# Kernel optimization log

Hardware: AMD Instinct MI355X
Metric: run time of the kernel (lower is better)

## Reference

```python
import jax, jax.numpy as jnp
import numpy as np

K = 16
EPS = 1e-5
NEG_SLOPE = 0.2


def leaky(x):
    return jnp.where(x > 0, x, NEG_SLOPE * x)


def batchnorm_train(x, gamma, beta):
    # x: [B, D]; training-mode BN with biased variance (torch semantics)
    mean = jnp.mean(x, axis=0)
    var = jnp.mean((x - mean) ** 2, axis=0)
    return (x - mean) * jax.lax.rsqrt(var + EPS) * gamma + beta


def setup_inputs() -> dict:
    key = jax.random.key(0)
    ks = jax.random.split(key, 20)
    N, M, D = 30000, 8000, 16
    s = lambda fan_in: 1.0 / np.sqrt(fan_in)
    inp = {
        "xyz": jax.random.normal(ks[0], (N, 3), jnp.float32),
        "atom_xyz": jax.random.normal(ks[1], (M, 3), jnp.float32),
        "atom_types": jax.random.normal(ks[2], (M, D), jnp.float32),
        "Wt1": jax.random.uniform(ks[3], (D, D), jnp.float32, -s(D), s(D)),
        "bt1": jax.random.uniform(ks[4], (D,), jnp.float32, -s(D), s(D)),
        "Wt2": jax.random.uniform(ks[5], (D, D), jnp.float32, -s(D), s(D)),
        "bt2": jax.random.uniform(ks[6], (D,), jnp.float32, -s(D), s(D)),
        "Wt3": jax.random.uniform(ks[7], (D, D), jnp.float32, -s(D), s(D)),
        "bt3": jax.random.uniform(ks[8], (D,), jnp.float32, -s(D), s(D)),
        # embed: conv1 Linear(D+1, D), conv2 Linear(D, D), conv3 Linear(2D, D)
        "W1": jax.random.uniform(ks[9], (D + 1, D), jnp.float32, -s(D + 1), s(D + 1)),
        "b1": jax.random.uniform(ks[10], (D,), jnp.float32, -s(D + 1), s(D + 1)),
        "W2": jax.random.uniform(ks[11], (D, D), jnp.float32, -s(D), s(D)),
        "b2": jax.random.uniform(ks[12], (D,), jnp.float32, -s(D), s(D)),
        "W3": jax.random.uniform(ks[13], (2 * D, D), jnp.float32, -s(2 * D), s(2 * D)),
        "b3": jax.random.uniform(ks[14], (D,), jnp.float32, -s(2 * D), s(2 * D)),
        # batchnorm affine params
        "g1": jnp.ones((D,), jnp.float32),
        "be1": jnp.zeros((D,), jnp.float32),
        "g2": jnp.ones((D,), jnp.float32),
        "be2": jnp.zeros((D,), jnp.float32),
    }
    return inp


def reference(xyz, atom_xyz, atom_types,
              Wt1, bt1, Wt2, bt2, Wt3, bt3,
              W1, b1, W2, b2, W3, b3, g1, be1, g2, be2):
    N, D = xyz.shape[0], atom_types.shape[1]

    # transform_types MLP on atom features: [M, D]
    t = leaky(atom_types @ Wt1 + bt1)
    t = leaky(t @ Wt2 + bt2)
    t = leaky(t @ Wt3 + bt3)

    # kNN: squared distances via GEMM expansion (avoids [N,M,3])
    d2 = (jnp.sum(xyz ** 2, axis=1, keepdims=True)
          + jnp.sum(atom_xyz ** 2, axis=1)[None, :]
          - 2.0 * xyz @ atom_xyz.T)                      # [N, M]
    _, idx = jax.lax.top_k(-d2, K)                       # [N, K] nearest atoms

    # gather neighbor coords, recompute exact squared dists (as in source)
    y_ik = atom_xyz[idx]                                 # [N, K, 3]
    dists = jnp.sum((xyz[:, None, :] - y_ik) ** 2, axis=-1)  # [N, K]

    feat = jnp.concatenate([t[idx], (1.0 / dists)[..., None]], axis=-1)  # [N,K,D+1]

    # conv1 -> leaky -> bn1 -> sum-pool
    fx = feat @ W1 + b1                                  # [N, K, D]
    fx = batchnorm_train(leaky(fx).reshape(-1, D), g1, be1).reshape(N, K, D)
    fx1 = fx.sum(axis=1)                                 # [N, D]

    # conv2 -> leaky -> bn2 -> sum-pool
    fx = fx @ W2 + b2
    fx = batchnorm_train(leaky(fx).reshape(-1, D), g2, be2).reshape(N, K, D)
    fx2 = fx.sum(axis=1)                                 # [N, D]

    return jnp.concatenate([fx1, fx2], axis=-1) @ W3 + b3  # [N, D]
```

## Files before the change

### kernel.cpp

```cpp
#include <hip/hip_runtime.h>

#define N_PTS   30000
#define M_ATOMS 8000
#define D       16
#define KNN     16
#define NGRP    125
#define EPS     1e-5f
#define SLOPE   0.2f
#define BN_COUNT 480000.0f

typedef unsigned long long ull;

__device__ __forceinline__ float leaky(float x) { return x > 0.f ? x : SLOPE * x; }

__device__ __forceinline__ unsigned fkey(float f) {
  unsigned u = __float_as_uint(f);
  return u ^ ((u & 0x80000000u) ? 0xFFFFFFFFu : 0x80000000u);
}
__device__ __forceinline__ float unfkey(unsigned e) {
  unsigned u = (e & 0x80000000u) ? (e ^ 0x80000000u) : ~e;
  return __uint_as_float(u);
}

#define DPPSTEP32(v, CTRL) {                                                   \
  unsigned t_ = (unsigned)__builtin_amdgcn_update_dpp(-1, (int)(v), CTRL, 0xF, 0xF, false); \
  (v) = t_ < (v) ? t_ : (v); }

__device__ __forceinline__ unsigned wmin32d(unsigned v) {
  DPPSTEP32(v, 0x111); DPPSTEP32(v, 0x112); DPPSTEP32(v, 0x114);
  DPPSTEP32(v, 0x118); DPPSTEP32(v, 0x142); DPPSTEP32(v, 0x143);
  return (unsigned)__builtin_amdgcn_readlane((int)v, 63);
}

__device__ __forceinline__ void cswap(ull& a, ull& b) {
  ull mn = a < b ? a : b, mx = a < b ? b : a;
  a = mn; b = mx;
}

__device__ __forceinline__ int morton_cell(float x, float y, float z) {
  int cx = min(max((int)floorf((x + 4.f) * 2.f), 0), 15);
  int cy = min(max((int)floorf((y + 4.f) * 2.f), 0), 15);
  int cz = min(max((int)floorf((z + 4.f) * 2.f), 0), 15);
  int c = 0;
#pragma unroll
  for (int b = 0; b < 4; ++b)
    c |= (((cx>>b)&1) << (3*b)) | (((cy>>b)&1) << (3*b+1)) | (((cz>>b)&1) << (3*b+2));
  return c;
}

#define LAYER(IN, OUT, W, B)                                        \
  _Pragma("unroll") for (int j = 0; j < 16; ++j) {                  \
    float acc = B[j];                                               \
    _Pragma("unroll") for (int i = 0; i < 16; ++i)                  \
      acc = fmaf(IN[i], W[i*16+j], acc);                            \
    OUT[j] = leaky(acc);                                            \
  }

__global__ void __launch_bounds__(256) kA_prep(
    const float* __restrict__ atom_xyz, const float* __restrict__ atom_types,
    const float* __restrict__ Wt1, const float* __restrict__ bt1,
    const float* __restrict__ Wt2, const float* __restrict__ bt2,
    const float* __restrict__ Wt3, const float* __restrict__ bt3,
    const float* __restrict__ W1, const float* __restrict__ b1,
    float* __restrict__ tu_out, float4* __restrict__ atoms4s,
    int* __restrict__ origid, float4* __restrict__ bounds,
    float* __restrict__ gstats) {
  int tid = threadIdx.x;
  if (blockIdx.x == 0) {
    __shared__ int h0[4096], h1[4096];
    __shared__ unsigned bmn[375], bmx[375];
    for (int i = tid; i < 4096; i += 256) { h0[i] = 0; }
    for (int i = tid; i < 375; i += 256) { bmn[i] = 0xFFFFFFFFu; bmx[i] = 0u; }
    for (int i = tid; i < 288; i += 256) gstats[i] = 0.f;
    __syncthreads();
    for (int r = 0; r < 32; ++r) {
      int m = r*256 + tid;
      if (m < M_ATOMS) {
        int c = morton_cell(atom_xyz[m*3], atom_xyz[m*3+1], atom_xyz[m*3+2]);
        atomicAdd(&h0[c], 1);
      }
    }
    __syncthreads();
    int* src = h0; int* dst = h1;
    for (int off = 1; off < 4096; off <<= 1) {
      for (int i = tid; i < 4096; i += 256) {
        int v = src[i];
        if (i >= off) v += src[i-off];
        dst[i] = v;
      }
      __syncthreads();
      int* t = src; src = dst; dst = t;
    }
    for (int i = tid; i < 4096; i += 256) dst[i] = i ? src[i-1] : 0;
    __syncthreads();
    for (int r = 0; r < 32; ++r) {
      int m = r*256 + tid;
      if (m < M_ATOMS) {
        float x = atom_xyz[m*3], y = atom_xyz[m*3+1], z = atom_xyz[m*3+2];
        int c = morton_cell(x, y, z);
        int pos = atomicAdd(&dst[c], 1);
        atoms4s[pos] = make_float4(x, y, z, fmaf(x,x, fmaf(y,y, z*z)));
        origid[pos] = m;
        int g = pos >> 6;
        atomicMin(&bmn[g],     fkey(x)); atomicMax(&bmx[g],     fkey(x));
        atomicMin(&bmn[125+g], fkey(y)); atomicMax(&bmx[125+g], fkey(y));
        atomicMin(&bmn[250+g], fkey(z)); atomicMax(&bmx[250+g], fkey(z));
      }
    }
    __syncthreads();
    if (tid < NGRP) {
      bounds[2*tid]   = make_float4(unfkey(bmn[tid]), unfkey(bmn[125+tid]),
                                    unfkey(bmn[250+tid]), 0.f);
      bounds[2*tid+1] = make_float4(unfkey(bmx[tid]), unfkey(bmx[125+tid]),
                                    unfkey(bmx[250+tid]), 0.f);
    }
  } else {
    __shared__ float w1[256], w2[256], w3[256], wc[256];
    __shared__ float bb1[16], bb2[16], bb3[16], bbc[16];
    w1[tid] = Wt1[tid]; w2[tid] = Wt2[tid]; w3[tid] = Wt3[tid]; wc[tid] = W1[tid];
    if (tid < 16) { bb1[tid] = bt1[tid]; bb2[tid] = bt2[tid];
                    bb3[tid] = bt3[tid]; bbc[tid] = b1[tid]; }
    __syncthreads();
    int m = (blockIdx.x - 1) * 256 + tid;
    if (m >= M_ATOMS) return;
    float u[16], v[16];
    const float4* tp = (const float4*)(atom_types + (size_t)m*16);
    float4 q0 = tp[0], q1 = tp[1], q2 = tp[2], q3 = tp[3];
    u[0]=q0.x; u[1]=q0.y; u[2]=q0.z; u[3]=q0.w;
    u[4]=q1.x; u[5]=q1.y; u[6]=q1.z; u[7]=q1.w;
    u[8]=q2.x; u[9]=q2.y; u[10]=q2.z; u[11]=q2.w;
    u[12]=q3.x; u[13]=q3.y; u[14]=q3.z; u[15]=q3.w;
    LAYER(u, v, w1, bb1);
    LAYER(v, u, w2, bb2);
    LAYER(u, v, w3, bb3);
    float up[16];
#pragma unroll
    for (int j = 0; j < 16; ++j) {
      float acc = bbc[j];
#pragma unroll
      for (int i = 0; i < 16; ++i) acc = fmaf(v[i], wc[i*16+j], acc);
      up[j] = acc;
    }
    float4* op = (float4*)(tu_out + (size_t)m*16);
    op[0] = make_float4(up[0], up[1], up[2], up[3]);
    op[1] = make_float4(up[4], up[5], up[6], up[7]);
    op[2] = make_float4(up[8], up[9], up[10], up[11]);
    op[3] = make_float4(up[12], up[13], up[14], up[15]);
  }
}

__global__ void __launch_bounds__(256) k2_knn(
    const float* __restrict__ xyz, const float4* __restrict__ atoms4s,
    const int* __restrict__ origid, const float4* __restrict__ bounds,
    const float* __restrict__ atom_xyz, const float* __restrict__ tu,
    const float* __restrict__ W1,
    int2* __restrict__ pairs, float* __restrict__ gstats) {
  __shared__ float sbuf[4*16*20];
  int tid = threadIdx.x;
  int lane = tid & 63;
  int wid = tid >> 6;
  int n = blockIdx.x * 4 + wid;

  float px = xyz[n*3+0], py = xyz[n*3+1], pz = xyz[n*3+2];
  float x2 = fmaf(px,px, fmaf(py,py, pz*pz));

  unsigned ea, eb = 0xFFFFFFFFu;
  {
    int g = lane;
    float4 mn = bounds[2*g], mx = bounds[2*g+1];
    float dx = fmaxf(fmaxf(mn.x - px, px - mx.x), 0.f);
    float dy = fmaxf(fmaxf(mn.y - py, py - mx.y), 0.f);
    float dz = fmaxf(fmaxf(mn.z - pz, pz - mx.z), 0.f);
    float lb = fmaf(dx,dx, fmaf(dy,dy, dz*dz)) * 0.999f - 1e-4f;
    ea = (fkey(lb) & 0xFFFFFF00u) | (unsigned)g;
  }
  if (lane + 64 < NGRP) {
    int g = lane + 64;
    float4 mn = bounds[2*g], mx = bounds[2*g+1];
    float dx = fmaxf(fmaxf(mn.x - px, px - mx.x), 0.f);
    float dy = fmaxf(fmaxf(mn.y - py, py - mx.y), 0.f);
    float dz = fmaxf(fmaxf(mn.z - pz, pz - mx.z), 0.f);
    float lb = fmaf(dx,dx, fmaf(dy,dy, dz*dz)) * 0.999f - 1e-4f;
    eb = (fkey(lb) & 0xFFFFFF00u) | (unsigned)g;
  }
  unsigned cur = ea < eb ? ea : eb;
  unsigned bak = ea < eb ? eb : ea;

  int gs[4];
#pragma unroll
  for (int r = 0; r < 4; ++r) {
    unsigned m = wmin32d(cur);
    bool own = (cur == m);
    cur = own ? bak : cur;
    bak = own ? 0xFFFFFFFFu : bak;
    gs[r] = (int)(m & 0xFFu);
  }

  float4 A[4]; int OI[4];
#pragma unroll
  for (int r = 0; r < 4; ++r) {
    int base = gs[r] << 6;
    A[r]  = atoms4s[base + lane];
    OI[r] = origid [base + lane];
  }
  ull E[4];
#pragma unroll
  for (int r = 0; r < 4; ++r) {
    float dotp = fmaf(px,A[r].x, fmaf(py,A[r].y, pz*A[r].z));
    float d2 = (x2 + A[r].w) - 2.f*dotp;
    E[r] = ((ull)fkey(d2) << 32) | (unsigned)OI[r];
  }
  cswap(E[0],E[1]); cswap(E[2],E[3]); cswap(E[0],E[2]);
  cswap(E[1],E[3]); cswap(E[1],E[2]);
  unsigned cf0 = (unsigned)(E[0] >> 32), ci0 = (unsigned)E[0];
  unsigned cf1 = (unsigned)(E[1] >> 32), ci1 = (unsigned)E[1];
  unsigned cf2 = (unsigned)(E[2] >> 32), ci2 = (unsigned)E[2];
  unsigned cf3 = (unsigned)(E[3] >> 32), ci3 = (unsigned)E[3];

  ull res = ~0ull;
  unsigned mf = 0, mi = 0;
  for (int r = 0; r < KNN; ++r) {
    mf = wmin32d(cf0);
    ull ball = __ballot(cf0 == mf);
    if (__popcll(ball) == 1) {
      int srcl = (int)(__ffsll(ball) - 1);
      mi = (unsigned)__builtin_amdgcn_readlane((int)ci0, srcl);
    } else {
      unsigned cand = (cf0 == mf) ? ci0 : 0xFFFFFFFFu;
      mi = wmin32d(cand);
    }
    bool own = (cf0 == mf) && (ci0 == mi);
    if (lane == r) res = (((ull)mf) << 32) | mi;
    cf0 = own ? cf1 : cf0; cf1 = own ? cf2 : cf1;
    cf2 = own ? cf3 : cf2; cf3 = own ? 0xFFFFFFFFu : cf3;
    ci0 = own ? ci1 : ci0; ci1 = own ? ci2 : ci1;
    ci2 = own ? ci3 : ci2; ci3 = own ? 0xFFFFFFFFu : ci3;
  }
  ull lv = res;
  ull thresh = (((ull)mf) << 32) | mi;

  for (int it = 0; it < NGRP - 4; ++it) {
    unsigned m = wmin32d(cur);
    if ((m & 0xFFFFFF00u) >= (unsigned)(thresh >> 32)) break;
    bool own = (cur == m);
    cur = own ? bak : cur;
    bak = own ? 0xFFFFFFFFu : bak;
    int base = (int)(m & 0xFFu) << 6;

    float4 a = atoms4s[base + lane];
    int oi2 = origid[base + lane];
    float dotp = fmaf(px,a.x, fmaf(py,a.y, pz*a.z));
    float d2 = (x2 + a.w) - 2.f*dotp;
    ull key = ((ull)fkey(d2) << 32) | (unsigned)oi2;

    ull mk = __ballot(key < thresh);
    while (mk) {
      int src = (int)(__ffsll(mk) - 1);
      mk &= mk - 1;
      unsigned klo = (unsigned)__builtin_amdgcn_readlane((int)(unsigned)key, src);
      unsigned khi = (unsigned)__builtin_amdgcn_readlane((int)(unsigned)(key >> 32), src);
      ull kc = ((ull)khi << 32) | klo;
      if (kc < thresh) {
        bool ins = (lane < KNN) && (kc < lv);
        unsigned pvlo = (unsigned)__builtin_amdgcn_update_dpp(0, (int)(unsigned)lv,        0x111, 0xF, 0xF, false);
        unsigned pvhi = (unsigned)__builtin_amdgcn_update_dpp(0, (int)(unsigned)(lv>>32), 0x111, 0xF, 0xF, false);
        int pins      =           __builtin_amdgcn_update_dpp(0, ins ? 1 : 0,              0x111, 0xF, 0xF, false);
        if (ins) lv = pins ? (((ull)pvhi << 32) | pvlo) : kc;
        unsigned tlo = (unsigned)__builtin_amdgcn_readlane((int)(unsigned)lv, KNN-1);
        unsigned thi = (unsigned)__builtin_amdgcn_readlane((int)(unsigned)(lv >> 32), KNN-1);
        thresh = ((ull)thi << 32) | tlo;
      }
    }
  }

  int oi = (int)(unsigned)(lv & 0xFFFFFFFFull);
  float iv = 0.f;
  if (lane < KNN) {
    float bx = atom_xyz[oi*3+0], by = atom_xyz[oi*3+1], bz = atom_xyz[oi*3+2];
    float dx = px - bx, dy = py - by, dz = pz - bz;
    float dd = fmaf(dx,dx, fmaf(dy,dy, dz*dz));
    iv = 1.f / dd;
    pairs[n*KNN + lane] = make_int2(oi, __float_as_int(iv));

    const float4* up4 = (const float4*)(tu + (size_t)oi*16);
    float4 u0 = up4[0], u1 = up4[1], u2 = up4[2], u3 = up4[3];
    float4* row = (float4*)&sbuf[(wid*16 + lane)*20];
    float4 w;
    w.x = leaky(fmaf(iv, W1[256+ 0], u0.x)); w.y = leaky(fmaf(iv, W1[256+ 1], u0.y));
    w.z = leaky(fmaf(iv, W1[256+ 2], u0.z)); w.w = leaky(fmaf(iv, W1[256+ 3], u0.w));
    row[0] = w;
    w.x = leaky(fmaf(iv, W1[256+ 4], u1.x)); w.y = leaky(fmaf(iv, W1[256+ 5], u1.y));
    w.z = leaky(fmaf(iv, W1[256+ 6], u1.z)); w.w = leaky(fmaf(iv, W1[256+ 7], u1.w));
    row[1] = w;
    w.x = leaky(fmaf(iv, W1[256+ 8], u2.x)); w.y = leaky(fmaf(iv, W1[256+ 9], u2.y));
    w.z = leaky(fmaf(iv, W1[256+10], u2.z)); w.w = leaky(fmaf(iv, W1[256+11], u2.w));
    row[2] = w;
    w.x = leaky(fmaf(iv, W1[256+12], u3.x)); w.y = leaky(fmaf(iv, W1[256+13], u3.y));
    w.z = leaky(fmaf(iv, W1[256+14], u3.z)); w.w = leaky(fmaf(iv, W1[256+15], u3.w));
    row[3] = w;
  }
  __syncthreads();
  {
    int ch = tid & 15, grp = tid >> 4;
    float S = 0.f, Q = 0.f;
#pragma unroll
    for (int i = 0; i < 4; ++i) {
      float v = sbuf[(grp*4 + i)*20 + ch];
      S += v; Q += v*v;
    }
    __syncthreads();
    sbuf[grp*20 + ch] = S;
    sbuf[400 + grp*20 + ch] = Q;
  }
  __syncthreads();
  if (tid < 32) {
    int ch = tid & 15;
    int off = (tid < 16) ? 0 : 400;
    float s = 0.f;
#pragma unroll
    for (int g = 0; g < 16; ++g) s += sbuf[off + g*20 + ch];
    atomicAdd(&gstats[(blockIdx.x & 7)*32 + tid], s);
  }
}

__device__ __forceinline__ void a1_row(const float* __restrict__ tu, int idx,
                                       float iv, const float* wiv, float* a) {
  const float4* up = (const float4*)(tu + (size_t)idx*16);
  float4 r0 = up[0], r1 = up[1], r2 = up[2], r3 = up[3];
  float u[16];
  u[0]=r0.x; u[1]=r0.y; u[2]=r0.z; u[3]=r0.w;
  u[4]=r1.x; u[5]=r1.y; u[6]=r1.z; u[7]=r1.w;
  u[8]=r2.x; u[9]=r2.y; u[10]=r2.z; u[11]=r2.w;
  u[12]=r3.x; u[13]=r3.y; u[14]=r3.z; u[15]=r3.w;
#pragma unroll
  for (int j = 0; j < 16; ++j) a[j] = leaky(fmaf(iv, wiv[j], u[j]));
}

__global__ void __launch_bounds__(256, 4) k4_main(
    const int2* __restrict__ pairs, const float* __restrict__ tu,
    const float* __restrict__ W1,
    const float* __restrict__ W2, const float* __restrict__ b2,
    const float* __restrict__ g1, const float* __restrict__ be1,
    float* __restrict__ fx1_out, float* __restrict__ s2_out,
    float* __restrict__ gstats) {
  __shared__ float wiv[16], w2s[256], b2s[16];
  __shared__ float sc1[16], sh1[16];
  __shared__ float buf[16*16*17];
  int tid = threadIdx.x;
  w2s[tid] = W2[tid];
  if (tid < 16) { wiv[tid] = W1[256 + tid]; b2s[tid] = b2[tid]; }
  if (tid < 16) {
    float s1 = 0.f, q1 = 0.f;
#pragma unroll
    for (int c = 0; c < 8; ++c) { s1 += gstats[c*32 + tid]; q1 += gstats[c*32 + 16 + tid]; }
    float mean = s1 * (1.f/BN_COUNT);
    float var  = q1 * (1.f/BN_COUNT) - mean*mean;
    float sC = g1[tid] / sqrtf(var + EPS);
    sc1[tid] = sC;
    sh1[tid] = be1[tid] - mean * sC;
  }
  __syncthreads();

  int g = blockIdx.x * 256 + tid;
  int p = tid >> 4, k = tid & 15;
  int2 pr = pairs[g];
  int idx = pr.x;
  float iv = __int_as_float(pr.y);
  float h[16], a2[16];
  a1_row(tu, idx, iv, wiv, h);
#pragma unroll
  for (int j = 0; j < 16; ++j) h[j] = fmaf(h[j], sc1[j], sh1[j]);
#pragma unroll
  for (int j = 0; j < 16; ++j) {
    float accj = b2s[j];
#pragma unroll
    for (int i = 0; i < 16; ++i) accj = fmaf(h[i], w2s[i*16+j], accj);
    a2[j] = leaky(accj);
  }

  float* myrow = &buf[(p*16 + k)*17];
  int p2 = tid >> 4, j2 = tid & 15;
#pragma unroll
  for (int j = 0; j < 16; ++j) myrow[j] = h[j];
  __syncthreads();
  {
    float s = 0.f;
#pragma unroll
    for (int kk = 0; kk < 16; ++kk) s += buf[(p2*16+kk)*17 + j2];
    fx1_out[(size_t)blockIdx.x*256 + tid] = s;
  }
  __syncthreads();
#pragma unroll
  for (int j = 0; j < 16; ++j) myrow[j] = a2[j];
  __syncthreads();
  float s2v = 0.f;
#pragma unroll
  for (int kk = 0; kk < 16; ++kk) s2v += buf[(p2*16+kk)*17 + j2];
  s2_out[(size_t)blockIdx.x*256 + tid] = s2v;
  __syncthreads();
#pragma unroll
  for (int j = 0; j < 16; ++j) myrow[j] = a2[j]*a2[j];
  __syncthreads();
  float q2v = 0.f;
#pragma unroll
  for (int kk = 0; kk < 16; ++kk) q2v += buf[(p2*16+kk)*17 + j2];
  __syncthreads();
  buf[p2*17 + j2] = s2v;
  buf[289 + p2*17 + j2] = q2v;
  __syncthreads();
  if (tid < 16) {
    float t1 = 0.f, t2 = 0.f;
#pragma unroll
    for (int pp = 0; pp < 16; ++pp) { t1 += buf[pp*17 + tid]; t2 += buf[289 + pp*17 + tid]; }
    atomicAdd(&gstats[256 + tid], t1);
    atomicAdd(&gstats[272 + tid], t2);
  }
}

__global__ void __launch_bounds__(256) k5_final(
    const float* __restrict__ fx1_in, const float* __restrict__ s2_in,
    const float* __restrict__ gstats,
    const float* __restrict__ W3, const float* __restrict__ b3,
    const float* __restrict__ g2, const float* __restrict__ be2,
    float* __restrict__ out) {
  __shared__ float w[512], bb[16], sc2[16], sh2[16];
  int tid = threadIdx.x;
  w[tid] = W3[tid]; w[256+tid] = W3[256+tid];
  if (tid < 16) {
    bb[tid] = b3[tid];
    float mean = gstats[256+tid] * (1.f/BN_COUNT);
    float var  = gstats[272+tid] * (1.f/BN_COUNT) - mean*mean;
    float s = g2[tid] / sqrtf(var + EPS);
    sc2[tid] = s;
    sh2[tid] = be2[tid] - mean * s;
  }
  __syncthreads();
  int n = blockIdx.x * 256 + tid;
  if (n >= N_PTS) return;

  const float4* f1p = (const float4*)(fx1_in + (size_t)n*16);
  const float4* f2p = (const float4*)(s2_in  + (size_t)n*16);
  float4 x0=f1p[0], x1=f1p[1], x2=f1p[2], x3=f1p[3];
  float4 y0=f2p[0], y1=f2p[1], y2=f2p[2], y3=f2p[3];
  float f1[16] = {x0.x,x0.y,x0.z,x0.w, x1.x,x1.y,x1.z,x1.w,
                  x2.x,x2.y,x2.z,x2.w, x3.x,x3.y,x3.z,x3.w};
  float f2[16] = {y0.x,y0.y,y0.z,y0.w, y1.x,y1.y,y1.z,y1.w,
                  y2.x,y2.y,y2.z,y2.w, y3.x,y3.y,y3.z,y3.w};
#pragma unroll
  for (int i = 0; i < 16; ++i) f2[i] = fmaf(sc2[i], f2[i], 16.f * sh2[i]);

  float4* op = (float4*)(out + (size_t)n*16);
  float o[16];
#pragma unroll
  for (int j = 0; j < 16; ++j) {
    float accj = bb[j];
#pragma unroll
    for (int i = 0; i < 16; ++i) accj = fmaf(f1[i], w[i*16+j], accj);
#pragma unroll
    for (int i = 0; i < 16; ++i) accj = fmaf(f2[i], w[(16+i)*16+j], accj);
    o[j] = accj;
  }
  op[0] = make_float4(o[0], o[1], o[2], o[3]);
  op[1] = make_float4(o[4], o[5], o[6], o[7]);
  op[2] = make_float4(o[8], o[9], o[10], o[11]);
  op[3] = make_float4(o[12], o[13], o[14], o[15]);
}

extern "C" void kernel_launch(void* const* d_in, const int* in_sizes, int n_in,
                              void* d_out, int out_size, void* d_ws, size_t ws_size,
                              hipStream_t stream) {
  const float* xyz        = (const float*)d_in[0];
  const float* atom_xyz   = (const float*)d_in[1];
  const float* atom_types = (const float*)d_in[2];
  const float* Wt1 = (const float*)d_in[3];  const float* bt1 = (const float*)d_in[4];
  const float* Wt2 = (const float*)d_in[5];  const float* bt2 = (const float*)d_in[6];
  const float* Wt3 = (const float*)d_in[7];  const float* bt3 = (const float*)d_in[8];
  const float* W1  = (const float*)d_in[9];  const float* b1  = (const float*)d_in[10];
  const float* W2  = (const float*)d_in[11]; const float* b2  = (const float*)d_in[12];
  const float* W3  = (const float*)d_in[13]; const float* b3  = (const float*)d_in[14];
  const float* g1  = (const float*)d_in[15]; const float* be1 = (const float*)d_in[16];
  const float* g2  = (const float*)d_in[17]; const float* be2 = (const float*)d_in[18];
  float* out = (float*)d_out;

  float* ws = (float*)d_ws;
  float*  tu       = ws;
  int2*   pairs    = (int2*)(ws + 128000);
  float*  fx1      = ws + 1088000;
  float*  s2       = ws + 1568000;
  float*  gstats   = ws + 2048000;
  float4* atoms4s  = (float4*)(ws + 1088000);
  int*    origid   = (int*)(ws + 1120000);
  float4* bounds   = (float4*)(ws + 1128000);

  kA_prep<<<33, 256, 0, stream>>>(atom_xyz, atom_types, Wt1, bt1, Wt2, bt2,
                                  Wt3, bt3, W1, b1, tu, atoms4s, origid,
                                  bounds, gstats);
  k2_knn<<<7500, 256, 0, stream>>>(xyz, atoms4s, origid, bounds, atom_xyz,
                                   tu, W1, pairs, gstats);
  k4_main<<<1875, 256, 0, stream>>>(pairs, tu, W1, W2, b2, g1, be1,
                                    fx1, s2, gstats);
  k5_final<<<118, 256, 0, stream>>>(fx1, s2, gstats, W3, b3, g2, be2, out);
}
```

Baseline: 235.7 us.

## Split serial single-block atom binning into parallel multi-kernel histogram, scan, scatter, bounds

The atom counting-sort preprocessing previously ran entirely in one 256-thread block (histogram, scan, scatter, per-group bounds via atomics) alongside the MLP blocks. It is now split across several kernels: a zeroing kernel, the MLP fused with a global-atomic histogram, a 1024-thread scan, a parallel scatter, and a wave-reduction bounds kernel. This removes the long serial tail of the single binning block but adds four extra kernel launches and their inter-kernel gaps.

```diff
diff --git a/kernel.cpp b/kernel.cpp
--- a/kernel.cpp
+++ b/kernel.cpp
@@ -17,10 +17,6 @@
   unsigned u = __float_as_uint(f);
   return u ^ ((u & 0x80000000u) ? 0xFFFFFFFFu : 0x80000000u);
 }
-__device__ __forceinline__ float unfkey(unsigned e) {
-  unsigned u = (e & 0x80000000u) ? (e ^ 0x80000000u) : ~e;
-  return __uint_as_float(u);
-}
 
 #define DPPSTEP32(v, CTRL) {                                                   \
   unsigned t_ = (unsigned)__builtin_amdgcn_update_dpp(-1, (int)(v), CTRL, 0xF, 0xF, false); \
@@ -46,6 +42,13 @@
   for (int b = 0; b < 4; ++b)
     c |= (((cx>>b)&1) << (3*b)) | (((cy>>b)&1) << (3*b+1)) | (((cz>>b)&1) << (3*b+2));
   return c;
+}
+
+__global__ void __launch_bounds__(256) kZ_zero(int* __restrict__ bins,
+                                               float* __restrict__ gstats) {
+  int i = blockIdx.x * 256 + threadIdx.x;
+  if (i < 4096) bins[i] = 0;
+  else if (i - 4096 < 288) gstats[i - 4096] = 0.f;
 }
 
 #define LAYER(IN, OUT, W, B)                                        \
@@ -56,96 +59,101 @@
     OUT[j] = leaky(acc);                                            \
   }
 
-__global__ void __launch_bounds__(256) kA_prep(
+__global__ void __launch_bounds__(256) kA_mlp_hist(
     const float* __restrict__ atom_xyz, const float* __restrict__ atom_types,
     const float* __restrict__ Wt1, const float* __restrict__ bt1,
     const float* __restrict__ Wt2, const float* __restrict__ bt2,
     const float* __restrict__ Wt3, const float* __restrict__ bt3,
     const float* __restrict__ W1, const float* __restrict__ b1,
-    float* __restrict__ tu_out, float4* __restrict__ atoms4s,
-    int* __restrict__ origid, float4* __restrict__ bounds,
-    float* __restrict__ gstats) {
+    float* __restrict__ tu_out, int* __restrict__ bins) {
+  __shared__ float w1[256], w2[256], w3[256], wc[256];
+  __shared__ float bb1[16], bb2[16], bb3[16], bbc[16];
   int tid = threadIdx.x;
-  if (blockIdx.x == 0) {
-    __shared__ int h0[4096], h1[4096];
-    __shared__ unsigned bmn[375], bmx[375];
-    for (int i = tid; i < 4096; i += 256) { h0[i] = 0; }
-    for (int i = tid; i < 375; i += 256) { bmn[i] = 0xFFFFFFFFu; bmx[i] = 0u; }
-    for (int i = tid; i < 288; i += 256) gstats[i] = 0.f;
-    __syncthreads();
-    for (int r = 0; r < 32; ++r) {
-      int m = r*256 + tid;
-      if (m < M_ATOMS) {
-        int c = morton_cell(atom_xyz[m*3], atom_xyz[m*3+1], atom_xyz[m*3+2]);
-        atomicAdd(&h0[c], 1);
-      }
+  w1[tid] = Wt1[tid]; w2[tid] = Wt2[tid]; w3[tid] = Wt3[tid]; wc[tid] = W1[tid];
+  if (tid < 16) { bb1[tid] = bt1[tid]; bb2[tid] = bt2[tid];
+                  bb3[tid] = bt3[tid]; bbc[tid] = b1[tid]; }
+  __syncthreads();
+  int m = blockIdx.x * 256 + tid;
+  if (m >= M_ATOMS) return;
+
+  int c = morton_cell(atom_xyz[m*3], atom_xyz[m*3+1], atom_xyz[m*3+2]);
+  atomicAdd(&bins[c], 1);
+
+  float u[16], v[16];
+  const float4* tp = (const float4*)(atom_types + (size_t)m*16);
+  float4 q0 = tp[0], q1 = tp[1], q2 = tp[2], q3 = tp[3];
+  u[0]=q0.x; u[1]=q0.y; u[2]=q0.z; u[3]=q0.w;
+  u[4]=q1.x; u[5]=q1.y; u[6]=q1.z; u[7]=q1.w;
+  u[8]=q2.x; u[9]=q2.y; u[10]=q2.z; u[11]=q2.w;
+  u[12]=q3.x; u[13]=q3.y; u[14]=q3.z; u[15]=q3.w;
+  LAYER(u, v, w1, bb1);
+  LAYER(v, u, w2, bb2);
+  LAYER(u, v, w3, bb3);
+  float up[16];
+#pragma unroll
+  for (int j = 0; j < 16; ++j) {
+    float acc = bbc[j];
+#pragma unroll
+    for (int i = 0; i < 16; ++i) acc = fmaf(v[i], wc[i*16+j], acc);
+    up[j] = acc;
+  }
+  float4* op = (float4*)(tu_out + (size_t)m*16);
+  op[0] = make_float4(up[0], up[1], up[2], up[3]);
+  op[1] = make_float4(up[4], up[5], up[6], up[7]);
+  op[2] = make_float4(up[8], up[9], up[10], up[11]);
+  op[3] = make_float4(up[12], up[13], up[14], up[15]);
+}
+
+__global__ void __launch_bounds__(1024) kB_scan(
+    const int* __restrict__ bins, int* __restrict__ cursors) {
+  __shared__ int h0[4096], h1[4096];
+  int tid = threadIdx.x;
+  for (int i = tid; i < 4096; i += 1024) h0[i] = bins[i];
+  __syncthreads();
+  int* src = h0; int* dst = h1;
+  for (int off = 1; off < 4096; off <<= 1) {
+    for (int i = tid; i < 4096; i += 1024) {
+      int v = src[i];
+      if (i >= off) v += src[i-off];
+      dst[i] = v;
     }
     __syncthreads();
-    int* src = h0; int* dst = h1;
-    for (int off = 1; off < 4096; off <<= 1) {
-      for (int i = tid; i < 4096; i += 256) {
-        int v = src[i];
-        if (i >= off) v += src[i-off];
-        dst[i] = v;
-      }
-      __syncthreads();
-      int* t = src; src = dst; dst = t;
-    }
-    for (int i = tid; i < 4096; i += 256) dst[i] = i ? src[i-1] : 0;
-    __syncthreads();
-    for (int r = 0; r < 32; ++r) {
-      int m = r*256 + tid;
-      if (m < M_ATOMS) {
-        float x = atom_xyz[m*3], y = atom_xyz[m*3+1], z = atom_xyz[m*3+2];
-        int c = morton_cell(x, y, z);
-        int pos = atomicAdd(&dst[c], 1);
-        atoms4s[pos] = make_float4(x, y, z, fmaf(x,x, fmaf(y,y, z*z)));
-        origid[pos] = m;
-        int g = pos >> 6;
-        atomicMin(&bmn[g],     fkey(x)); atomicMax(&bmx[g],     fkey(x));
-        atomicMin(&bmn[125+g], fkey(y)); atomicMax(&bmx[125+g], fkey(y));
-        atomicMin(&bmn[250+g], fkey(z)); atomicMax(&bmx[250+g], fkey(z));
-      }
-    }
-    __syncthreads();
-    if (tid < NGRP) {
-      bounds[2*tid]   = make_float4(unfkey(bmn[tid]), unfkey(bmn[125+tid]),
-                                    unfkey(bmn[250+tid]), 0.f);
-      bounds[2*tid+1] = make_float4(unfkey(bmx[tid]), unfkey(bmx[125+tid]),
-                                    unfkey(bmx[250+tid]), 0.f);
-    }
-  } else {
-    __shared__ float w1[256], w2[256], w3[256], wc[256];
-    __shared__ float bb1[16], bb2[16], bb3[16], bbc[16];
-    w1[tid] = Wt1[tid]; w2[tid] = Wt2[tid]; w3[tid] = Wt3[tid]; wc[tid] = W1[tid];
-    if (tid < 16) { bb1[tid] = bt1[tid]; bb2[tid] = bt2[tid];
-                    bb3[tid] = bt3[tid]; bbc[tid] = b1[tid]; }
-    __syncthreads();
-    int m = (blockIdx.x - 1) * 256 + tid;
-    if (m >= M_ATOMS) return;
-    float u[16], v[16];
-    const float4* tp = (const float4*)(atom_types + (size_t)m*16);
-    float4 q0 = tp[0], q1 = tp[1], q2 = tp[2], q3 = tp[3];
-    u[0]=q0.x; u[1]=q0.y; u[2]=q0.z; u[3]=q0.w;
-    u[4]=q1.x; u[5]=q1.y; u[6]=q1.z; u[7]=q1.w;
-    u[8]=q2.x; u[9]=q2.y; u[10]=q2.z; u[11]=q2.w;
-    u[12]=q3.x; u[13]=q3.y; u[14]=q3.z; u[15]=q3.w;
-    LAYER(u, v, w1, bb1);
-    LAYER(v, u, w2, bb2);
-    LAYER(u, v, w3, bb3);
-    float up[16];
-#pragma unroll
-    for (int j = 0; j < 16; ++j) {
-      float acc = bbc[j];
-#pragma unroll
-      for (int i = 0; i < 16; ++i) acc = fmaf(v[i], wc[i*16+j], acc);
-      up[j] = acc;
-    }
-    float4* op = (float4*)(tu_out + (size_t)m*16);
-    op[0] = make_float4(up[0], up[1], up[2], up[3]);
-    op[1] = make_float4(up[4], up[5], up[6], up[7]);
-    op[2] = make_float4(up[8], up[9], up[10], up[11]);
-    op[3] = make_float4(up[12], up[13], up[14], up[15]);
+    int* t = src; src = dst; dst = t;
+  }
+  for (int i = tid; i < 4096; i += 1024) cursors[i] = i ? src[i-1] : 0;
+}
+
+__global__ void __launch_bounds__(256) kC_scatter(
+    const float* __restrict__ atom_xyz, int* __restrict__ cursors,
+    float4* __restrict__ atoms4s, int* __restrict__ origid) {
+  int m = blockIdx.x * 256 + threadIdx.x;
+  if (m >= M_ATOMS) return;
+  float x = atom_xyz[m*3], y = atom_xyz[m*3+1], z = atom_xyz[m*3+2];
+  int c = morton_cell(x, y, z);
+  int pos = atomicAdd(&cursors[c], 1);
+  atoms4s[pos] = make_float4(x, y, z, fmaf(x,x, fmaf(y,y, z*z)));
+  origid[pos] = m;
+}
+
+__global__ void __launch_bounds__(256) k_bounds(
+    const float4* __restrict__ atoms4s, float4* __restrict__ bounds) {
+  int lane = threadIdx.x & 63;
+  int g = blockIdx.x * 4 + (threadIdx.x >> 6);
+  if (g >= NGRP) return;
+  float4 a = atoms4s[(g << 6) + lane];
+  float mnx=a.x, mny=a.y, mnz=a.z, mxx=a.x, mxy=a.y, mxz=a.z;
+#pragma unroll
+  for (int off = 32; off; off >>= 1) {
+    mnx = fminf(mnx, __shfl_xor(mnx, off, 64));
+    mny = fminf(mny, __shfl_xor(mny, off, 64));
+    mnz = fminf(mnz, __shfl_xor(mnz, off, 64));
+    mxx = fmaxf(mxx, __shfl_xor(mxx, off, 64));
+    mxy = fmaxf(mxy, __shfl_xor(mxy, off, 64));
+    mxz = fmaxf(mxz, __shfl_xor(mxz, off, 64));
+  }
+  if (lane == 0) {
+    bounds[2*g]   = make_float4(mnx, mny, mnz, 0.f);
+    bounds[2*g+1] = make_float4(mxx, mxy, mxz, 0.f);
   }
 }
 
@@ -488,13 +496,18 @@
   float*  fx1      = ws + 1088000;
   float*  s2       = ws + 1568000;
   float*  gstats   = ws + 2048000;
+  int*    bins     = (int*)(ws + 2048288);
+  int*    cursors  = (int*)(ws + 2052384);
   float4* atoms4s  = (float4*)(ws + 1088000);
   int*    origid   = (int*)(ws + 1120000);
   float4* bounds   = (float4*)(ws + 1128000);
 
-  kA_prep<<<33, 256, 0, stream>>>(atom_xyz, atom_types, Wt1, bt1, Wt2, bt2,
-                                  Wt3, bt3, W1, b1, tu, atoms4s, origid,
-                                  bounds, gstats);
+  kZ_zero<<<18, 256, 0, stream>>>(bins, gstats);
+  kA_mlp_hist<<<32, 256, 0, stream>>>(atom_xyz, atom_types, Wt1, bt1, Wt2, bt2,
+                                      Wt3, bt3, W1, b1, tu, bins);
+  kB_scan<<<1, 1024, 0, stream>>>(bins, cursors);
+  kC_scatter<<<32, 256, 0, stream>>>(atom_xyz, cursors, atoms4s, origid);
+  k_bounds<<<32, 256, 0, stream>>>(atoms4s, bounds);
   k2_knn<<<7500, 256, 0, stream>>>(xyz, atoms4s, origid, bounds, atom_xyz,
                                    tu, W1, pairs, gstats);
   k4_main<<<1875, 256, 0, stream>>>(pairs, tu, W1, W2, b2, g1, be1,
```

Result: faster. 212.8 us (-9.7%).

## Split atom binning into a 1024-thread scan kernel and a parallel scatter kernel

Applied to the files above, without the earlier changes.

The single-block histogram, scan and scatter stage that ran inside the prep kernel is split in two. A 1024-thread single-block kernel builds the Morton histogram and exclusive scan into global cursors. A 32-block kernel then scatters atoms with global atomics and computes per-group bounds through global atomicMin/Max, fused with the type MLP. This removes the serial 256-thread block that bounded the prep stage. In exchange it adds a kernel launch, and the bounds are stored as encoded keys that the kNN kernel decodes itself.

```diff
diff --git a/kernel.cpp b/kernel.cpp
--- a/kernel.cpp
+++ b/kernel.cpp
@@ -48,6 +48,35 @@
   return c;
 }
 
+__global__ void __launch_bounds__(1024) kB_hist_scan(
+    const float* __restrict__ atom_xyz, int* __restrict__ cursors,
+    float* __restrict__ gstats, unsigned* __restrict__ benc) {
+  __shared__ int h0[4096], h1[4096];
+  int tid = threadIdx.x;
+  for (int i = tid; i < 4096; i += 1024) h0[i] = 0;
+  if (tid < 288) gstats[tid] = 0.f;
+  if (tid >= 288 && tid < 663) benc[tid - 288] = 0xFFFFFFFFu;
+  if (tid >= 663 && tid < 1024) benc[tid - 288] = 0u;
+  if (tid < 14) benc[736 + tid] = 0u;
+  __syncthreads();
+  for (int m = tid; m < M_ATOMS; m += 1024) {
+    int c = morton_cell(atom_xyz[m*3], atom_xyz[m*3+1], atom_xyz[m*3+2]);
+    atomicAdd(&h0[c], 1);
+  }
+  __syncthreads();
+  int* src = h0; int* dst = h1;
+  for (int off = 1; off < 4096; off <<= 1) {
+    for (int i = tid; i < 4096; i += 1024) {
+      int v = src[i];
+      if (i >= off) v += src[i-off];
+      dst[i] = v;
+    }
+    __syncthreads();
+    int* t = src; src = dst; dst = t;
+  }
+  for (int i = tid; i < 4096; i += 1024) cursors[i] = i ? src[i-1] : 0;
+}
+
 #define LAYER(IN, OUT, W, B)                                        \
   _Pragma("unroll") for (int j = 0; j < 16; ++j) {                  \
     float acc = B[j];                                               \
@@ -56,102 +85,63 @@
     OUT[j] = leaky(acc);                                            \
   }
 
-__global__ void __launch_bounds__(256) kA_prep(
+__global__ void __launch_bounds__(256) kC_scatter_mlp(
     const float* __restrict__ atom_xyz, const float* __restrict__ atom_types,
     const float* __restrict__ Wt1, const float* __restrict__ bt1,
     const float* __restrict__ Wt2, const float* __restrict__ bt2,
     const float* __restrict__ Wt3, const float* __restrict__ bt3,
     const float* __restrict__ W1, const float* __restrict__ b1,
-    float* __restrict__ tu_out, float4* __restrict__ atoms4s,
-    int* __restrict__ origid, float4* __restrict__ bounds,
-    float* __restrict__ gstats) {
+    int* __restrict__ cursors, float4* __restrict__ atoms4s,
+    int* __restrict__ origid, unsigned* __restrict__ benc,
+    float* __restrict__ tu_out) {
+  __shared__ float w1[256], w2[256], w3[256], wc[256];
+  __shared__ float bb1[16], bb2[16], bb3[16], bbc[16];
   int tid = threadIdx.x;
-  if (blockIdx.x == 0) {
-    __shared__ int h0[4096], h1[4096];
-    __shared__ unsigned bmn[375], bmx[375];
-    for (int i = tid; i < 4096; i += 256) { h0[i] = 0; }
-    for (int i = tid; i < 375; i += 256) { bmn[i] = 0xFFFFFFFFu; bmx[i] = 0u; }
-    for (int i = tid; i < 288; i += 256) gstats[i] = 0.f;
-    __syncthreads();
-    for (int r = 0; r < 32; ++r) {
-      int m = r*256 + tid;
-      if (m < M_ATOMS) {
-        int c = morton_cell(atom_xyz[m*3], atom_xyz[m*3+1], atom_xyz[m*3+2]);
-        atomicAdd(&h0[c], 1);
-      }
-    }
-    __syncthreads();
-    int* src = h0; int* dst = h1;
-    for (int off = 1; off < 4096; off <<= 1) {
-      for (int i = tid; i < 4096; i += 256) {
-        int v = src[i];
-        if (i >= off) v += src[i-off];
-        dst[i] = v;
-      }
-      __syncthreads();
-      int* t = src; src = dst; dst = t;
-    }
-    for (int i = tid; i < 4096; i += 256) dst[i] = i ? src[i-1] : 0;
-    __syncthreads();
-    for (int r = 0; r < 32; ++r) {
-      int m = r*256 + tid;
-      if (m < M_ATOMS) {
-        float x = atom_xyz[m*3], y = atom_xyz[m*3+1], z = atom_xyz[m*3+2];
-        int c = morton_cell(x, y, z);
-        int pos = atomicAdd(&dst[c], 1);
-        atoms4s[pos] = make_float4(x, y, z, fmaf(x,x, fmaf(y,y, z*z)));
-        origid[pos] = m;
-        int g = pos >> 6;
-        atomicMin(&bmn[g],     fkey(x)); atomicMax(&bmx[g],     fkey(x));
-        atomicMin(&bmn[125+g], fkey(y)); atomicMax(&bmx[125+g], fkey(y));
-        atomicMin(&bmn[250+g], fkey(z)); atomicMax(&bmx[250+g], fkey(z));
-      }
-    }
-    __syncthreads();
-    if (tid < NGRP) {
-      bounds[2*tid]   = make_float4(unfkey(bmn[tid]), unfkey(bmn[125+tid]),
-                                    unfkey(bmn[250+tid]), 0.f);
-      bounds[2*tid+1] = make_float4(unfkey(bmx[tid]), unfkey(bmx[125+tid]),
-                                    unfkey(bmx[250+tid]), 0.f);
-    }
-  } else {
-    __shared__ float w1[256], w2[256], w3[256], wc[256];
-    __shared__ float bb1[16], bb2[16], bb3[16], bbc[16];
-    w1[tid] = Wt1[tid]; w2[tid] = Wt2[tid]; w3[tid] = Wt3[tid]; wc[tid] = W1[tid];
-    if (tid < 16) { bb1[tid] = bt1[tid]; bb2[tid] = bt2[tid];
-                    bb3[tid] = bt3[tid]; bbc[tid] = b1[tid]; }
-    __syncthreads();
-    int m = (blockIdx.x - 1) * 256 + tid;
-    if (m >= M_ATOMS) return;
-    float u[16], v[16];
-    const float4* tp = (const float4*)(atom_types + (size_t)m*16);
-    float4 q0 = tp[0], q1 = tp[1], q2 = tp[2], q3 = tp[3];
-    u[0]=q0.x; u[1]=q0.y; u[2]=q0.z; u[3]=q0.w;
-    u[4]=q1.x; u[5]=q1.y; u[6]=q1.z; u[7]=q1.w;
-    u[8]=q2.x; u[9]=q2.y; u[10]=q2.z; u[11]=q2.w;
-    u[12]=q3.x; u[13]=q3.y; u[14]=q3.z; u[15]=q3.w;
-    LAYER(u, v, w1, bb1);
-    LAYER(v, u, w2, bb2);
-    LAYER(u, v, w3, bb3);
-    float up[16];
-#pragma unroll
-    for (int j = 0; j < 16; ++j) {
-      float acc = bbc[j];
-#pragma unroll
-      for (int i = 0; i < 16; ++i) acc = fmaf(v[i], wc[i*16+j], acc);
-      up[j] = acc;
-    }
-    float4* op = (float4*)(tu_out + (size_t)m*16);
-    op[0] = make_float4(up[0], up[1], up[2], up[3]);
-    op[1] = make_float4(up[4], up[5], up[6], up[7]);
-    op[2] = make_float4(up[8], up[9], up[10], up[11]);
-    op[3] = make_float4(up[12], up[13], up[14], up[15]);
-  }
+  w1[tid] = Wt1[tid]; w2[tid] = Wt2[tid]; w3[tid] = Wt3[tid]; wc[tid] = W1[tid];
+  if (tid < 16) { bb1[tid] = bt1[tid]; bb2[tid] = bt2[tid];
+                  bb3[tid] = bt3[tid]; bbc[tid] = b1[tid]; }
+  __syncthreads();
+  int m = blockIdx.x * 256 + tid;
+  if (m >= M_ATOMS) return;
+
+  float x = atom_xyz[m*3], y = atom_xyz[m*3+1], z = atom_xyz[m*3+2];
+  int c = morton_cell(x, y, z);
+  int pos = atomicAdd(&cursors[c], 1);
+  atoms4s[pos] = make_float4(x, y, z, fmaf(x,x, fmaf(y,y, z*z)));
+  origid[pos] = m;
+  int g = pos >> 6;
+  atomicMin(&benc[g],       fkey(x)); atomicMax(&benc[375+g], fkey(x));
+  atomicMin(&benc[125+g],   fkey(y)); atomicMax(&benc[500+g], fkey(y));
+  atomicMin(&benc[250+g],   fkey(z)); atomicMax(&benc[625+g], fkey(z));
+
+  float u[16], v[16];
+  const float4* tp = (const float4*)(atom_types + (size_t)m*16);
+  float4 q0 = tp[0], q1 = tp[1], q2 = tp[2], q3 = tp[3];
+  u[0]=q0.x; u[1]=q0.y; u[2]=q0.z; u[3]=q0.w;
+  u[4]=q1.x; u[5]=q1.y; u[6]=q1.z; u[7]=q1.w;
+  u[8]=q2.x; u[9]=q2.y; u[10]=q2.z; u[11]=q2.w;
+  u[12]=q3.x; u[13]=q3.y; u[14]=q3.z; u[15]=q3.w;
+  LAYER(u, v, w1, bb1);
+  LAYER(v, u, w2, bb2);
+  LAYER(u, v, w3, bb3);
+  float up[16];
+#pragma unroll
+  for (int j = 0; j < 16; ++j) {
+    float acc = bbc[j];
+#pragma unroll
+    for (int i = 0; i < 16; ++i) acc = fmaf(v[i], wc[i*16+j], acc);
+    up[j] = acc;
+  }
+  float4* op = (float4*)(tu_out + (size_t)m*16);
+  op[0] = make_float4(up[0], up[1], up[2], up[3]);
+  op[1] = make_float4(up[4], up[5], up[6], up[7]);
+  op[2] = make_float4(up[8], up[9], up[10], up[11]);
+  op[3] = make_float4(up[12], up[13], up[14], up[15]);
 }
 
 __global__ void __launch_bounds__(256) k2_knn(
     const float* __restrict__ xyz, const float4* __restrict__ atoms4s,
-    const int* __restrict__ origid, const float4* __restrict__ bounds,
+    const int* __restrict__ origid, const unsigned* __restrict__ benc,
     const float* __restrict__ atom_xyz, const float* __restrict__ tu,
     const float* __restrict__ W1,
     int2* __restrict__ pairs, float* __restrict__ gstats) {
@@ -167,19 +157,21 @@
   unsigned ea, eb = 0xFFFFFFFFu;
   {
     int g = lane;
-    float4 mn = bounds[2*g], mx = bounds[2*g+1];
-    float dx = fmaxf(fmaxf(mn.x - px, px - mx.x), 0.f);
-    float dy = fmaxf(fmaxf(mn.y - py, py - mx.y), 0.f);
-    float dz = fmaxf(fmaxf(mn.z - pz, pz - mx.z), 0.f);
+    float mnx = unfkey(benc[g]),     mny = unfkey(benc[125+g]), mnz = unfkey(benc[250+g]);
+    float mxx = unfkey(benc[375+g]), mxy = unfkey(benc[500+g]), mxz = unfkey(benc[625+g]);
+    float dx = fmaxf(fmaxf(mnx - px, px - mxx), 0.f);
+    float dy = fmaxf(fmaxf(mny - py, py - mxy), 0.f);
+    float dz = fmaxf(fmaxf(mnz - pz, pz - mxz), 0.f);
     float lb = fmaf(dx,dx, fmaf(dy,dy, dz*dz)) * 0.999f - 1e-4f;
     ea = (fkey(lb) & 0xFFFFFF00u) | (unsigned)g;
   }
   if (lane + 64 < NGRP) {
     int g = lane + 64;
-    float4 mn = bounds[2*g], mx = bounds[2*g+1];
-    float dx = fmaxf(fmaxf(mn.x - px, px - mx.x), 0.f);
-    float dy = fmaxf(fmaxf(mn.y - py, py - mx.y), 0.f);
-    float dz = fmaxf(fmaxf(mn.z - pz, pz - mx.z), 0.f);
+    float mnx = unfkey(benc[g]),     mny = unfkey(benc[125+g]), mnz = unfkey(benc[250+g]);
+    float mxx = unfkey(benc[375+g]), mxy = unfkey(benc[500+g]), mxz = unfkey(benc[625+g]);
+    float dx = fmaxf(fmaxf(mnx - px, px - mxx), 0.f);
+    float dy = fmaxf(fmaxf(mny - py, py - mxy), 0.f);
+    float dz = fmaxf(fmaxf(mnz - pz, pz - mxz), 0.f);
     float lb = fmaf(dx,dx, fmaf(dy,dy, dz*dz)) * 0.999f - 1e-4f;
     eb = (fkey(lb) & 0xFFFFFF00u) | (unsigned)g;
   }
@@ -483,19 +475,21 @@
   float* out = (float*)d_out;
 
   float* ws = (float*)d_ws;
-  float*  tu       = ws;
-  int2*   pairs    = (int2*)(ws + 128000);
-  float*  fx1      = ws + 1088000;
-  float*  s2       = ws + 1568000;
-  float*  gstats   = ws + 2048000;
-  float4* atoms4s  = (float4*)(ws + 1088000);
-  int*    origid   = (int*)(ws + 1120000);
-  float4* bounds   = (float4*)(ws + 1128000);
-
-  kA_prep<<<33, 256, 0, stream>>>(atom_xyz, atom_types, Wt1, bt1, Wt2, bt2,
-                                  Wt3, bt3, W1, b1, tu, atoms4s, origid,
-                                  bounds, gstats);
-  k2_knn<<<7500, 256, 0, stream>>>(xyz, atoms4s, origid, bounds, atom_xyz,
+  float*    tu      = ws;
+  int2*     pairs   = (int2*)(ws + 128000);
+  float*    fx1     = ws + 1088000;
+  float*    s2      = ws + 1568000;
+  float*    gstats  = ws + 2048000;
+  int*      cursors = (int*)(ws + 2048288);
+  unsigned* benc    = (unsigned*)(ws + 2052384);
+  float4*   atoms4s = (float4*)(ws + 1088000);
+  int*      origid  = (int*)(ws + 1120000);
+
+  kB_hist_scan<<<1, 1024, 0, stream>>>(atom_xyz, cursors, gstats, benc);
+  kC_scatter_mlp<<<32, 256, 0, stream>>>(atom_xyz, atom_types, Wt1, bt1,
+                                         Wt2, bt2, Wt3, bt3, W1, b1,
+                                         cursors, atoms4s, origid, benc, tu);
+  k2_knn<<<7500, 256, 0, stream>>>(xyz, atoms4s, origid, benc, atom_xyz,
                                    tu, W1, pairs, gstats);
   k4_main<<<1875, 256, 0, stream>>>(pairs, tu, W1, W2, b2, g1, be1,
                                     fx1, s2, gstats);
```

Result: faster. 215.5 us (-8.6%).
